# Performance work log

Measured on AMD Instinct MI355X. Metric: run time of the kernel, lower is better.

The kernel has to match this reference:

```python
import jax, jax.numpy as jnp
import numpy as np

B_, C_, H_, W_ = 8, 128, 64, 64
OUT_ = 128
D_MODEL = C_ // 4        # 32, per-chunk channels fed to Mamba
D_STATE = 16
D_CONV = 4
D_INNER = 2 * D_MODEL    # expand=2 -> 64
DT_RANK = max(1, -(-D_MODEL // 16))  # ceil(32/16)=2
SE_RED = 2


def _ln(x, g, b):
    m = x.mean(-1, keepdims=True)
    v = jnp.var(x, axis=-1, keepdims=True)
    return (x - m) / jnp.sqrt(v + 1e-5) * g + b


def _mamba(u, in_W, conv_W, conv_b, xproj_W, dt_W, dt_b, A_log, D_p, out_W):
    # u: (B, L, d_model)
    Bsz, L, _ = u.shape
    xz = u @ in_W.T                                   # (B,L,2*d_inner)
    x, z = jnp.split(xz, 2, axis=-1)
    # causal depthwise conv1d along L
    xc = jnp.swapaxes(x, 1, 2)                        # (B,d_inner,L)
    xc = jax.lax.conv_general_dilated(
        xc, conv_W, (1,), [(D_CONV - 1, 0)],
        feature_group_count=D_INNER,
        dimension_numbers=('NCH', 'OIH', 'NCH'))
    x = jax.nn.silu(jnp.swapaxes(xc + conv_b[None, :, None], 1, 2))
    x_dbl = x @ xproj_W.T                             # (B,L,dt_rank+2*d_state)
    dt, Bm, Cm = jnp.split(x_dbl, [DT_RANK, DT_RANK + D_STATE], axis=-1)
    dt = jax.nn.softplus(dt @ dt_W.T + dt_b)          # (B,L,d_inner)
    A = -jnp.exp(A_log)                               # (d_inner,d_state)
    dA = jnp.exp(dt[..., None] * A)                   # (B,L,d_inner,d_state)
    dBu = dt[..., None] * Bm[:, :, None, :] * x[..., None]

    def step(h, inp):
        dA_t, dBu_t, C_t = inp
        h = dA_t * h + dBu_t                          # (B,d_inner,d_state)
        return h, jnp.einsum('bds,bs->bd', h, C_t)

    h0 = jnp.zeros((Bsz, D_INNER, D_STATE), dtype=x.dtype)
    _, ys = jax.lax.scan(step, h0, (jnp.swapaxes(dA, 0, 1), jnp.swapaxes(dBu, 0, 1), jnp.swapaxes(Cm, 0, 1)))
    y = jnp.swapaxes(ys, 0, 1) + x * D_p
    y = y * jax.nn.silu(z)
    return y @ out_W.T


def _branch(xi, skip_scale, se_W1, se_W2, mp):
    M1 = _mamba(xi, *mp)                              # (B,L,c)
    M2 = skip_scale * xi
    # SE: adaptive avg-pool over spatial == mean over tokens; cat over channels
    y = jnp.concatenate([M1, M2], axis=-1).mean(axis=1)   # (B,2c)
    y = jax.nn.sigmoid(jax.nn.relu(y @ se_W1.T) @ se_W2.T)
    g1, g2 = jnp.split(y, 2, axis=-1)
    return g1[:, None, :] * M1 + g2[:, None, :] * M2


def _pvm(x, norm_g, norm_b, proj_W, proj_b, skip_scale, se_W1, se_W2,
         in_W, conv_W, conv_b, xproj_W, dt_W, dt_b, A_log, D_p, out_W):
    B, C, H, W = x.shape
    L = H * W
    xf = jnp.swapaxes(x.reshape(B, C, L), 1, 2)       # (B,L,C)
    xn = _ln(xf, norm_g, norm_b)
    mp = (in_W, conv_W, conv_b, xproj_W, dt_W, dt_b, A_log, D_p, out_W)
    outs = [_branch(c, skip_scale, se_W1, se_W2, mp) for c in jnp.split(xn, 4, axis=2)]
    xm = jnp.concatenate(outs, axis=2)                # (B,L,C)
    xm = _ln(xm, norm_g, norm_b)
    xm = xm @ proj_W.T + proj_b                       # (B,L,out)
    return jnp.swapaxes(xm, 1, 2).reshape(B, proj_W.shape[0], H, W)


def setup_inputs():
    key = jax.random.key(0)
    ks = jax.random.split(key, 10)
    p = {}
    p['x'] = jax.random.normal(ks[0], (B_, C_, H_, W_), jnp.float32)
    p['norm_g'] = jnp.ones((C_,), jnp.float32)
    p['norm_b'] = jnp.zeros((C_,), jnp.float32)
    p['proj_W'] = jax.random.normal(ks[1], (OUT_, C_), jnp.float32) * 0.05
    p['proj_b'] = jnp.zeros((OUT_,), jnp.float32)
    p['skip_scale'] = jnp.ones((1,), jnp.float32)
    p['se_W1'] = jax.random.normal(ks[2], (SE_RED, 2 * D_MODEL), jnp.float32) * 0.1
    p['se_W2'] = jax.random.normal(ks[3], (2 * D_MODEL, SE_RED), jnp.float32) * 0.1
    p['in_W'] = jax.random.normal(ks[4], (2 * D_INNER, D_MODEL), jnp.float32) * 0.1
    p['conv_W'] = jax.random.normal(ks[5], (D_INNER, 1, D_CONV), jnp.float32) * 0.2
    p['conv_b'] = jnp.zeros((D_INNER,), jnp.float32)
    p['xproj_W'] = jax.random.normal(ks[6], (DT_RANK + 2 * D_STATE, D_INNER), jnp.float32) * 0.1
    p['dt_W'] = jax.random.normal(ks[7], (D_INNER, DT_RANK), jnp.float32) * 0.1
    p['dt_b'] = jnp.full((D_INNER,), -4.6, jnp.float32)  # softplus(-4.6) ~ 0.01 init dt
    p['A_log'] = jnp.log(jnp.broadcast_to(jnp.arange(1.0, D_STATE + 1.0, dtype=jnp.float32), (D_INNER, D_STATE)))
    p['D_p'] = jnp.ones((D_INNER,), jnp.float32)
    p['out_W'] = jax.random.normal(ks[8], (D_MODEL, D_INNER), jnp.float32) * 0.1
    return p


def reference(x, norm_g, norm_b, proj_W, proj_b, skip_scale, se_W1, se_W2,
              in_W, conv_W, conv_b, xproj_W, dt_W, dt_b, A_log, D_p, out_W):
    return _pvm(x, norm_g, norm_b, proj_W, proj_b, skip_scale, se_W1, se_W2,
                in_W, conv_W, conv_b, xproj_W, dt_W, dt_b, A_log, D_p, out_W)
```

## Files before the change

### kernel.cpp

```cpp
#include <hip/hip_runtime.h>
#include <math.h>

typedef _Float16 h16;

#define DEV static __device__ __forceinline__

constexpr int B_ = 8, C_ = 128, L_ = 4096, OUT_ = 128;
constexpr int NCH = 4, DM = 32, DS = 16, DI = 64;
constexpr int NI = 32;
constexpr int NSEG = 128;
constexpr int SL = L_ / NSEG;

DEV float sigmoidf_(float x) { return 1.f / (1.f + __expf(-x)); }
DEV float siluf_(float x) { return x * sigmoidf_(x); }
DEV float softplusf_(float x) { return (x > 20.f) ? x : __logf(1.f + __expf(x)); }

template <int CTRL>
DEV float dpp_add_(float x) {
  int v = __builtin_amdgcn_update_dpp(0, __float_as_int(x), CTRL, 0xf, 0xf, false);
  return x + __int_as_float(v);
}

typedef __attribute__((ext_vector_type(8))) _Float16 f16x8;
typedef __attribute__((ext_vector_type(4))) _Float16 f16x4;
typedef __attribute__((ext_vector_type(4))) float f32x4;

DEV void powladder_(float E, float* out) {
  float E2 = E * E;
  float E4 = E2 * E2;
  float E8 = E4 * E4;
  float E3 = E2 * E;
  out[0] = E;       out[1] = E2;      out[2] = E3;      out[3] = E4;
  out[4] = E4 * E;  out[5] = E4 * E2; out[6] = E4 * E3; out[7] = E8;
  out[8] = E8 * E;  out[9] = E8 * E2; out[10] = E8 * E3; out[11] = E8 * E4;
  out[12] = E8 * out[4]; out[13] = E8 * out[5]; out[14] = E8 * out[6];
  out[15] = E8 * E8;
}

__global__ __launch_bounds__(256) void k1_ln(const float* __restrict__ x,
                                             const float* __restrict__ gn,
                                             const float* __restrict__ bn,
                                             float* __restrict__ XN,
                                             float* __restrict__ SUMXN) {
  int bid = blockIdx.x;
  int b = bid >> 6, tile = bid & 63;
  int t0 = tile * 64;
  int tid = threadIdx.x;
  __shared__ float xT[128][65];
  __shared__ float gnS[128], bnS[128];
  __shared__ float red[256];
  if (tid < 128) { gnS[tid] = gn[tid]; bnS[tid] = bn[tid]; }
  for (int k = tid; k < 8192; k += 256) {
    int c = k >> 6, tt = k & 63;
    xT[c][tt] = x[((size_t)(b * C_ + c)) * L_ + t0 + tt];
  }
  __syncthreads();
  {
    int tok = tid >> 2, q = tid & 3;
    float s = 0.f, qq = 0.f;
#pragma unroll
    for (int j = 0; j < 32; ++j) {
      float v = xT[q + 4 * j][tok];
      s += v; qq += v * v;
    }
    s = dpp_add_<0xB1>(s); qq = dpp_add_<0xB1>(qq);
    s = dpp_add_<0x4E>(s); qq = dpp_add_<0x4E>(qq);
    float m = s * (1.f / 128.f);
    float var = qq * (1.f / 128.f) - m * m;
    float rs = rsqrtf(var + 1e-5f);
#pragma unroll
    for (int j = 0; j < 32; ++j) {
      int c = q + 4 * j;
      float v = xT[c][tok];
      xT[c][tok] = (v - m) * rs * gnS[c] + bnS[c];
    }
  }
  __syncthreads();
  float acc = 0.f;
  int cfix = tid & 127;
  for (int k = tid; k < 8192; k += 256) {
    int tt = k >> 7, c = k & 127;
    float v = xT[c][tt];
    XN[((size_t)(b * L_ + t0 + tt)) * C_ + c] = v;
    acc += v;
  }
  red[tid] = acc;
  __syncthreads();
  if (tid < 128) atomicAdd(&SUMXN[b * C_ + cfix], red[tid] + red[tid + 128]);
}

__global__ __launch_bounds__(256) void k2_prep(
    const float* __restrict__ in_W, const float* __restrict__ conv_W,
    const float* __restrict__ conv_b, const float* __restrict__ xproj_W,
    const float* __restrict__ dt_W, const float* __restrict__ dt_b,
    const float* __restrict__ XN, h16* __restrict__ SX2, h16* __restrict__ SDT2,
    h16* __restrict__ SB2, h16* __restrict__ SC2, h16* __restrict__ SZ2) {
  int bid = blockIdx.x;
  int i = bid >> 6, tile = bid & 63;
  int b = i >> 2, ch = i & 3;
  int t0 = tile * 64;
  int tid = threadIdx.x;
  int w = __builtin_amdgcn_readfirstlane(tid >> 6);
  int lane = tid & 63;

  __shared__ __attribute__((aligned(16))) union {
    struct {
      _Float16 uH[80][40];
      _Float16 w1H[64][40];
    } s;
    float xdS[64][36];
    _Float16 zL[64][88];
  } U;
  __shared__ __attribute__((aligned(16))) _Float16 preH[80][66];
  __shared__ __attribute__((aligned(16))) _Float16 xH[64][72];
  __shared__ __attribute__((aligned(16))) _Float16 w2H[48][72];
  __shared__ float convWS[64][4];
  __shared__ float dtWS[64][2];
  __shared__ float dtbS[64], cbS[64];

  convWS[tid >> 2][tid & 3] = conv_W[tid];
  if (tid < 128) dtWS[tid >> 1][tid & 1] = dt_W[tid];
  if (tid < 64) { dtbS[tid] = dt_b[tid]; cbS[tid] = conv_b[tid]; }
  const float* xn = XN + (size_t)b * L_ * C_ + ch * DM;
  for (int k = tid; k < 80 * 32; k += 256) {
    int r = k >> 5, c = k & 31;
    int tg = t0 - 3 + r;
    float v = (r < 67 && tg >= 0) ? xn[(size_t)tg * C_ + c] : 0.f;
    U.s.uH[r][c] = (_Float16)v;
  }
  for (int k = tid; k < 2048; k += 256) U.s.w1H[k >> 5][k & 31] = (_Float16)in_W[k];
  for (int k = tid; k < 48 * 64; k += 256) {
    int r = k >> 6, c = k & 63;
    w2H[r][c] = (r < 34) ? (_Float16)xproj_W[r * 64 + c] : (_Float16)0.f;
  }
  __syncthreads();

  int rsel = lane & 15, ksel = (lane >> 4) * 8;
  {
    int nt = w;
    f16x8 bf = *(const f16x8*)&U.s.w1H[nt * 16 + rsel][ksel];
    int row0q = (lane >> 4) << 2;
    int col = nt * 16 + rsel;
#pragma unroll
    for (int mt = 0; mt < 5; ++mt) {
      f16x8 af = *(const f16x8*)&U.s.uH[mt * 16 + rsel][ksel];
      f32x4 acc = {0.f, 0.f, 0.f, 0.f};
      acc = __builtin_amdgcn_mfma_f32_16x16x32_f16(af, bf, acc, 0, 0, 0);
      int row0 = mt * 16 + row0q;
#pragma unroll
      for (int r = 0; r < 4; ++r) preH[row0 + r][col] = (_Float16)acc[r];
    }
  }
  f32x4 zacc[4];
  {
    f16x8 bf = *(const f16x8*)&U.s.uH[3 + w * 16 + rsel][ksel];
#pragma unroll
    for (int mt = 0; mt < 4; ++mt) {
      const float* wp = in_W + (64 + mt * 16 + rsel) * 32 + ksel;
      float4 w0 = *(const float4*)wp;
      float4 w1 = *(const float4*)(wp + 4);
      f16x8 af;
      af[0] = (_Float16)w0.x; af[1] = (_Float16)w0.y;
      af[2] = (_Float16)w0.z; af[3] = (_Float16)w0.w;
      af[4] = (_Float16)w1.x; af[5] = (_Float16)w1.y;
      af[6] = (_Float16)w1.z; af[7] = (_Float16)w1.w;
      f32x4 acc = {0.f, 0.f, 0.f, 0.f};
      zacc[mt] = __builtin_amdgcn_mfma_f32_16x16x32_f16(af, bf, acc, 0, 0, 0);
    }
  }
  __syncthreads();

  h16* SXp = SX2 + ((size_t)i * L_ + t0) * DI;
  for (int k = tid; k < 4096; k += 256) {
    int r = k >> 6, d = k & 63;
    float v = cbS[d];
#pragma unroll
    for (int j = 0; j < 4; ++j) v = fmaf(convWS[d][j], (float)preH[r + j][d], v);
    v = siluf_(v);
    xH[r][d] = (_Float16)v;
    SXp[(size_t)r * DI + d] = (h16)v;
  }
  __syncthreads();

  {
    int mt = w;
    f16x8 a0 = *(const f16x8*)&xH[mt * 16 + rsel][ksel];
    f16x8 a1 = *(const f16x8*)&xH[mt * 16 + rsel][32 + ksel];
    int row0 = mt * 16 + ((lane >> 4) << 2);
#pragma unroll
    for (int nt = 0; nt < 3; ++nt) {
      f16x8 b0 = *(const f16x8*)&w2H[nt * 16 + rsel][ksel];
      f16x8 b1 = *(const f16x8*)&w2H[nt * 16 + rsel][32 + ksel];
      f32x4 acc = {0.f, 0.f, 0.f, 0.f};
      acc = __builtin_amdgcn_mfma_f32_16x16x32_f16(a0, b0, acc, 0, 0, 0);
      acc = __builtin_amdgcn_mfma_f32_16x16x32_f16(a1, b1, acc, 0, 0, 0);
      int col = nt * 16 + rsel;
      if (col < 34) {
#pragma unroll
        for (int r = 0; r < 4; ++r) U.xdS[row0 + r][col] = acc[r];
      }
    }
  }
  __syncthreads();

  h16* SDTp = SDT2 + ((size_t)i * L_ + t0) * DI;
  for (int k = tid; k < 4096; k += 256) {
    int d = k & 63, r = k >> 6;
    float raw = fmaf(U.xdS[r][0], dtWS[d][0], fmaf(U.xdS[r][1], dtWS[d][1], dtbS[d]));
    SDTp[(size_t)r * DI + d] = (h16)softplusf_(raw);
  }
  h16* SBp = SB2 + ((size_t)i * L_ + t0) * DS;
  h16* SCp = SC2 + ((size_t)i * L_ + t0) * DS;
  for (int k = tid; k < 1024; k += 256) {
    int s = k & 15, r = k >> 4;
    SBp[(size_t)r * DS + s] = (h16)U.xdS[r][2 + s];
    SCp[(size_t)r * DS + s] = (h16)U.xdS[r][18 + s];
  }
  __syncthreads();

  {
    int tok = w * 16 + rsel;
    int zq = (lane >> 4) << 2;
#pragma unroll
    for (int mt = 0; mt < 4; ++mt) {
      f16x4 pk;
#pragma unroll
      for (int r = 0; r < 4; ++r) pk[r] = (_Float16)siluf_(zacc[mt][r]);
      *(f16x4*)&U.zL[tok][mt * 16 + zq] = pk;
    }
  }
  __syncthreads();
  h16* SZp = SZ2 + ((size_t)i * L_ + t0) * DI;
  for (int k = tid; k < 512; k += 256) {
    int r = k >> 3, dblk = (k & 7) * 8;
    f16x8 v = *(const f16x8*)&U.zL[r][dblk];
    *(f16x8*)&SZp[(size_t)r * DI + dblk] = v;
  }
}

__global__ __launch_bounds__(256) void k3a_seg(
    const float* __restrict__ A_log, const h16* __restrict__ SDT2,
    const h16* __restrict__ SX2, const h16* __restrict__ SB2,
    float* __restrict__ Pp, float* __restrict__ Qp) {
  int bid = blockIdx.x;
  int i = bid >> 5, sg = bid & 31;
  int tid = threadIdx.x;
  int w = tid >> 6, lane = tid & 63;
  int seg = sg * 4 + w;
  int t0 = seg * SL;
  __shared__ float bS[4][SL][20];
  {
    int tk = lane & 31, hf = lane >> 5;
    const h16* pb = SB2 + ((size_t)i * L_ + t0 + tk) * DS + hf * 8;
    float4 r0 = *(const float4*)pb;
    const h16* h0p = (const h16*)&r0;
#pragma unroll
    for (int s = 0; s < 8; ++s) bS[w][tk][hf * 8 + s] = (float)h0p[s];
  }
  __syncthreads();
  float Av[16];
#pragma unroll
  for (int s = 0; s < 16; ++s) Av[s] = -__expf(A_log[lane * 16 + s]);
  float A0 = Av[0];
  bool okf = true;
#pragma unroll
  for (int s = 0; s < 16; ++s) okf &= fabsf(Av[s] - (float)(s + 1) * A0) <= 1e-4f * fabsf(Av[s]);
  int fastp = __all(okf ? 1 : 0);
  float h[16];
#pragma unroll
  for (int s = 0; s < 16; ++s) h[s] = 0.f;
  float sdt = 0.f;
  const h16* pdt = SDT2 + ((size_t)i * L_ + t0) * DI + lane;
  const h16* pxx = SX2 + ((size_t)i * L_ + t0) * DI + lane;
  float dtc = (float)pdt[0], xvc = (float)pxx[0];
  for (int t = 0; t < SL; ++t) {
    float dt = dtc, xv = xvc;
    if (t < SL - 1) { dtc = (float)pdt[(t + 1) * DI]; xvc = (float)pxx[(t + 1) * DI]; }
    float Bv[16];
    const float* row = &bS[w][t][0];
#pragma unroll
    for (int j = 0; j < 4; ++j) *(float4*)&Bv[4 * j] = *(const float4*)(row + 4 * j);
    float dtx = dt * xv;
    float dA[16];
    if (fastp) {
      powladder_(__expf(A0 * dt), dA);
    } else {
#pragma unroll
      for (int s = 0; s < 16; ++s) dA[s] = __expf(Av[s] * dt);
    }
#pragma unroll
    for (int s = 0; s < 16; ++s) h[s] = fmaf(dA[s], h[s], dtx * Bv[s]);
    sdt += dt;
  }
  float P[16];
  if (fastp) {
    powladder_(__expf(A0 * sdt), P);
  } else {
#pragma unroll
    for (int s = 0; s < 16; ++s) P[s] = __expf(Av[s] * sdt);
  }
  size_t base = (((size_t)i * DI + lane) * NSEG + seg) * DS;
#pragma unroll
  for (int j = 0; j < 4; ++j) {
    *(float4*)(Pp + base + 4 * j) = *(float4*)&P[4 * j];
    *(float4*)(Qp + base + 4 * j) = *(float4*)&h[4 * j];
  }
}

__global__ __launch_bounds__(256) void k3b_comb(float* __restrict__ Pp,
                                                const float* __restrict__ Qp) {
  int g = blockIdx.x * 256 + threadIdx.x;
  int s = g & 15;
  int r = g >> 4;
  size_t base = (size_t)r * NSEG * DS + s;
  float H = 0.f;
  for (int seg = 0; seg < NSEG; ++seg) {
    size_t a = base + (size_t)seg * DS;
    float P = Pp[a], Q = Qp[a];
    Pp[a] = H;
    H = fmaf(P, H, Q);
  }
}

__global__ __launch_bounds__(256) void k3c_scan(
    const float* __restrict__ A_log, const h16* __restrict__ SDT2,
    const h16* __restrict__ SX2, const h16* __restrict__ SB2,
    const h16* __restrict__ SC2, const h16* __restrict__ SZ2,
    const float* __restrict__ D_p, const float* __restrict__ H0p,
    h16* __restrict__ YS2, float* __restrict__ SUMYF) {
  int bid = blockIdx.x;
  int i = bid >> 5, sg = bid & 31;
  int tid = threadIdx.x;
  int w = tid >> 6, lane = tid & 63;
  int seg = sg * 4 + w;
  int t0 = seg * SL;
  __shared__ float rowS[4][SL][36];
  {
    int tk = lane & 31, hf = lane >> 5;
    const h16* p = (hf ? SC2 : SB2) + ((size_t)i * L_ + t0 + tk) * DS;
    float4 r0 = *(const float4*)p;
    float4 r1 = *(const float4*)(p + 8);
    const h16* hp0 = (const h16*)&r0;
    const h16* hp1 = (const h16*)&r1;
#pragma unroll
    for (int s = 0; s < 8; ++s) {
      rowS[w][tk][hf * 16 + s] = (float)hp0[s];
      rowS[w][tk][hf * 16 + 8 + s] = (float)hp1[s];
    }
  }
  __syncthreads();
  float Av[16];
#pragma unroll
  for (int s = 0; s < 16; ++s) Av[s] = -__expf(A_log[lane * 16 + s]);
  float A0 = Av[0];
  bool okf = true;
#pragma unroll
  for (int s = 0; s < 16; ++s) okf &= fabsf(Av[s] - (float)(s + 1) * A0) <= 1e-4f * fabsf(Av[s]);
  int fastp = __all(okf ? 1 : 0);
  float Dp = D_p[lane];
  float h[16];
  {
    size_t base = (((size_t)i * DI + lane) * NSEG + seg) * DS;
#pragma unroll
    for (int j = 0; j < 4; ++j) *(float4*)&h[4 * j] = *(const float4*)(H0p + base + 4 * j);
  }
  const h16* pdt = SDT2 + ((size_t)i * L_ + t0) * DI + lane;
  const h16* pxx = SX2 + ((size_t)i * L_ + t0) * DI + lane;
  const h16* pzz = SZ2 + ((size_t)i * L_ + t0) * DI + lane;
  h16* pys = YS2 + ((size_t)i * L_ + t0) * DI + lane;
  float dtc = (float)pdt[0], xvc = (float)pxx[0], zvc = (float)pzz[0];
  float sum = 0.f;
  for (int t = 0; t < SL; ++t) {
    float dt = dtc, xv = xvc, zv = zvc;
    if (t < SL - 1) {
      dtc = (float)pdt[(t + 1) * DI];
      xvc = (float)pxx[(t + 1) * DI];
      zvc = (float)pzz[(t + 1) * DI];
    }
    const float* row = &rowS[w][t][0];
    float Bv[16], Cv[16];
#pragma unroll
    for (int j = 0; j < 4; ++j) {
      *(float4*)&Bv[4 * j] = *(const float4*)(row + 4 * j);
      *(float4*)&Cv[4 * j] = *(const float4*)(row + 16 + 4 * j);
    }
    float dtx = dt * xv;
    float dA[16];
    if (fastp) {
      powladder_(__expf(A0 * dt), dA);
    } else {
#pragma unroll
      for (int s = 0; s < 16; ++s) dA[s] = __expf(Av[s] * dt);
    }
    float y0 = 0.f, y1 = 0.f, y2 = 0.f, y3 = 0.f;
#pragma unroll
    for (int s = 0; s < 16; s += 4) {
      h[s] = fmaf(dA[s], h[s], dtx * Bv[s]);       y0 = fmaf(h[s], Cv[s], y0);
      h[s + 1] = fmaf(dA[s + 1], h[s + 1], dtx * Bv[s + 1]); y1 = fmaf(h[s + 1], Cv[s + 1], y1);
      h[s + 2] = fmaf(dA[s + 2], h[s + 2], dtx * Bv[s + 2]); y2 = fmaf(h[s + 2], Cv[s + 2], y2);
      h[s + 3] = fmaf(dA[s + 3], h[s + 3], dtx * Bv[s + 3]); y3 = fmaf(h[s + 3], Cv[s + 3], y3);
    }
    float y = (y0 + y1) + (y2 + y3);
    float yf = fmaf(xv, Dp, y) * zv;
    pys[(size_t)t * DI] = (h16)yf;
    sum += yf;
  }
  atomicAdd(&SUMYF[i * DI + lane], sum);
}

__global__ __launch_bounds__(64) void k4_gates(
    const float* __restrict__ out_W, const float* __restrict__ se_W1,
    const float* __restrict__ se_W2, const float* __restrict__ skip_p,
    const float* __restrict__ SUMYF, const float* __restrict__ SUMXN,
    float* __restrict__ GATES) {
  int i = blockIdx.x;
  int b = i >> 2, ch = i & 3;
  int tid = threadIdx.x;
  __shared__ float syS[64], catS[64], seS[2];
  syS[tid] = SUMYF[i * DI + tid];
  __syncthreads();
  float invL = 1.f / (float)L_;
  if (tid < 32) {
    float acc = 0.f;
#pragma unroll
    for (int dd = 0; dd < 64; ++dd) acc = fmaf(syS[dd], out_W[tid * 64 + dd], acc);
    catS[tid] = acc * invL;
  } else {
    int c = tid - 32;
    catS[tid] = skip_p[0] * SUMXN[b * C_ + ch * DM + c] * invL;
  }
  __syncthreads();
  if (tid < 2) {
    float acc = 0.f;
#pragma unroll
    for (int k = 0; k < 64; ++k) acc = fmaf(catS[k], se_W1[tid * 64 + k], acc);
    seS[tid] = fmaxf(acc, 0.f);
  }
  __syncthreads();
  float gg = fmaf(seS[0], se_W2[tid * 2 + 0], seS[1] * se_W2[tid * 2 + 1]);
  GATES[i * DI + tid] = sigmoidf_(gg);
}

__global__ __launch_bounds__(256) void k5b_combine(
    const float* __restrict__ out_W, const float* __restrict__ skip_p,
    const float* __restrict__ GATES, const h16* __restrict__ YS2,
    float* __restrict__ XN) {
  int bid = blockIdx.x;
  int i = bid >> 6, tile = bid & 63;
  int b = i >> 2, ch = i & 3;
  int t0 = tile * 64;
  int tid = threadIdx.x;
  int w = __builtin_amdgcn_readfirstlane(tid >> 6);
  int lane = tid & 63;
  __shared__ __attribute__((aligned(16))) _Float16 yH[64][72];
  __shared__ __attribute__((aligned(16))) _Float16 owH[32][72];
  __shared__ float xnS[64][37];
  __shared__ float gS[64];
  if (tid < 64) gS[tid] = GATES[i * DI + tid];
  const h16* py = YS2 + ((size_t)i * L_ + t0) * DI;
  for (int k = tid; k < 512; k += 256) {
    int tt = k >> 3, dblk = (k & 7) * 8;
    *(f16x8*)&yH[tt][dblk] = *(const f16x8*)&py[(size_t)tt * DI + dblk];
  }
  for (int k = tid; k < 2048; k += 256) owH[k >> 6][k & 63] = (_Float16)out_W[k];
  float* xn = XN + (size_t)b * L_ * C_ + ch * DM;
  for (int k = tid; k < 2048; k += 256) {
    int tt = k >> 5, o = k & 31;
    xnS[tt][o] = xn[(size_t)(t0 + tt) * C_ + o];
  }
  __syncthreads();
  int rsel = lane & 15, ksel = (lane >> 4) * 8;
  float skip = skip_p[0];
  int mt = w;
  f16x8 a0 = *(const f16x8*)&yH[mt * 16 + rsel][ksel];
  f16x8 a1 = *(const f16x8*)&yH[mt * 16 + rsel][32 + ksel];
  int row0 = mt * 16 + ((lane >> 4) << 2);
#pragma unroll
  for (int nt = 0; nt < 2; ++nt) {
    f16x8 b0 = *(const f16x8*)&owH[nt * 16 + rsel][ksel];
    f16x8 b1 = *(const f16x8*)&owH[nt * 16 + rsel][32 + ksel];
    f32x4 acc = {0.f, 0.f, 0.f, 0.f};
    acc = __builtin_amdgcn_mfma_f32_16x16x32_f16(a0, b0, acc, 0, 0, 0);
    acc = __builtin_amdgcn_mfma_f32_16x16x32_f16(a1, b1, acc, 0, 0, 0);
    int o = nt * 16 + rsel;
    float g1 = gS[o], g2s = gS[32 + o] * skip;
#pragma unroll
    for (int r = 0; r < 4; ++r) {
      int tok = row0 + r;
      xnS[tok][o] = g1 * acc[r] + g2s * xnS[tok][o];
    }
  }
  __syncthreads();
  for (int k = tid; k < 2048; k += 256) {
    int tt = k >> 5, o = k & 31;
    xn[(size_t)(t0 + tt) * C_ + o] = xnS[tt][o];
  }
}

__global__ __launch_bounds__(256) void k6_ln_proj(
    const float* __restrict__ gn, const float* __restrict__ bn,
    const float* __restrict__ proj_W, const float* __restrict__ proj_b,
    const float* __restrict__ XN, float* __restrict__ out) {
  int bid = blockIdx.x;
  int b = bid >> 6, tile = bid & 63;
  int t0 = tile * 64;
  int tid = threadIdx.x;
  int w = __builtin_amdgcn_readfirstlane(tid >> 6);
  int lane = tid & 63;
  __shared__ __attribute__((aligned(16))) union {
    float xmS[64][132];
    _Float16 projH[128][136];
  } U;
  __shared__ __attribute__((aligned(16))) _Float16 xmH[64][136];
  __shared__ float gnS[128], bnS[128];
  if (tid < 128) { gnS[tid] = gn[tid]; bnS[tid] = bn[tid]; }
  const float* xm = XN + (size_t)b * L_ * C_;
  for (int k = tid; k < 8192; k += 256) {
    int tt = k >> 7, c = k & 127;
    U.xmS[tt][c] = xm[(size_t)(t0 + tt) * C_ + c];
  }
  __syncthreads();
  {
    int tok = tid >> 2, q = tid & 3;
    float s = 0.f, qq = 0.f;
#pragma unroll
    for (int j = 0; j < 32; ++j) {
      float v = U.xmS[tok][4 * j + q];
      s += v; qq += v * v;
    }
    s = dpp_add_<0xB1>(s); qq = dpp_add_<0xB1>(qq);
    s = dpp_add_<0x4E>(s); qq = dpp_add_<0x4E>(qq);
    float m = s * (1.f / 128.f);
    float var = qq * (1.f / 128.f) - m * m;
    float rs = rsqrtf(var + 1e-5f);
#pragma unroll
    for (int j = 0; j < 32; ++j) {
      int c = 4 * j + q;
      float v = U.xmS[tok][c];
      U.xmS[tok][c] = (v - m) * rs * gnS[c] + bnS[c];
    }
  }
  __syncthreads();
  for (int k = tid; k < 1024; k += 256) {
    int tt = k >> 4, cblk = (k & 15) * 8;
    float4 v0 = *(const float4*)&U.xmS[tt][cblk];
    float4 v1 = *(const float4*)&U.xmS[tt][cblk + 4];
    f16x8 hv;
    hv[0] = (_Float16)v0.x; hv[1] = (_Float16)v0.y;
    hv[2] = (_Float16)v0.z; hv[3] = (_Float16)v0.w;
    hv[4] = (_Float16)v1.x; hv[5] = (_Float16)v1.y;
    hv[6] = (_Float16)v1.z; hv[7] = (_Float16)v1.w;
    *(f16x8*)&xmH[tt][cblk] = hv;
  }
  __syncthreads();
  for (int k = tid; k < 2048; k += 256) {
    int o = k >> 4, cblk = (k & 15) * 8;
    const float* wp = proj_W + o * 128 + cblk;
    float4 v0 = *(const float4*)wp;
    float4 v1 = *(const float4*)(wp + 4);
    f16x8 hv;
    hv[0] = (_Float16)v0.x; hv[1] = (_Float16)v0.y;
    hv[2] = (_Float16)v0.z; hv[3] = (_Float16)v0.w;
    hv[4] = (_Float16)v1.x; hv[5] = (_Float16)v1.y;
    hv[6] = (_Float16)v1.z; hv[7] = (_Float16)v1.w;
    *(f16x8*)&U.projH[o][cblk] = hv;
  }
  __syncthreads();
  int rsel = lane & 15, ksel = (lane >> 4) * 8;
  int mt = w;
  f16x8 af[4];
#pragma unroll
  for (int kc = 0; kc < 4; ++kc)
    af[kc] = *(const f16x8*)&xmH[mt * 16 + rsel][kc * 32 + ksel];
  int row0 = mt * 16 + ((lane >> 4) << 2);
#pragma unroll
  for (int nt = 0; nt < 8; ++nt) {
    int o = nt * 16 + rsel;
    float pb = proj_b[o];
    f32x4 acc = {pb, pb, pb, pb};
#pragma unroll
    for (int kc = 0; kc < 4; ++kc) {
      f16x8 bf = *(const f16x8*)&U.projH[o][kc * 32 + ksel];
      acc = __builtin_amdgcn_mfma_f32_16x16x32_f16(af[kc], bf, acc, 0, 0, 0);
    }
    *(float4*)&out[((size_t)(b * OUT_ + o)) * L_ + t0 + row0] =
        make_float4(acc[0], acc[1], acc[2], acc[3]);
  }
}

extern "C" void kernel_launch(void* const* d_in, const int* in_sizes, int n_in,
                              void* d_out, int out_size, void* d_ws, size_t ws_size,
                              hipStream_t stream) {
  const float* x = (const float*)d_in[0];
  const float* norm_g = (const float*)d_in[1];
  const float* norm_b = (const float*)d_in[2];
  const float* proj_W = (const float*)d_in[3];
  const float* proj_b = (const float*)d_in[4];
  const float* skip = (const float*)d_in[5];
  const float* se_W1 = (const float*)d_in[6];
  const float* se_W2 = (const float*)d_in[7];
  const float* in_W = (const float*)d_in[8];
  const float* conv_W = (const float*)d_in[9];
  const float* conv_b = (const float*)d_in[10];
  const float* xproj_W = (const float*)d_in[11];
  const float* dt_W = (const float*)d_in[12];
  const float* dt_b = (const float*)d_in[13];
  const float* A_log = (const float*)d_in[14];
  const float* D_p = (const float*)d_in[15];
  const float* out_W = (const float*)d_in[16];
  float* out = (float*)d_out;

  float* XN = (float*)d_ws;
  float* SUMYF = XN + (size_t)B_ * L_ * C_;
  float* SUMXN = SUMYF + NI * DI;
  float* GATES = SUMXN + B_ * C_;
  float* Pp = GATES + NI * DI;
  float* Qp = Pp + (size_t)NI * DI * NSEG * DS;
  h16* YS2 = (h16*)(Qp + (size_t)NI * DI * NSEG * DS);
  h16* SX2 = YS2 + (size_t)NI * L_ * DI;
  h16* SDT2 = SX2 + (size_t)NI * L_ * DI;
  h16* SB2 = SDT2 + (size_t)NI * L_ * DI;
  h16* SC2 = SB2 + (size_t)NI * L_ * DS;
  h16* SZ2 = SC2 + (size_t)NI * L_ * DS;

  hipMemsetAsync(SUMYF, 0, (size_t)(NI * DI + B_ * C_) * sizeof(float), stream);
  k1_ln<<<B_ * 64, 256, 0, stream>>>(x, norm_g, norm_b, XN, SUMXN);
  k2_prep<<<NI * 64, 256, 0, stream>>>(in_W, conv_W, conv_b, xproj_W, dt_W, dt_b,
                                       XN, SX2, SDT2, SB2, SC2, SZ2);
  k3a_seg<<<NI * 32, 256, 0, stream>>>(A_log, SDT2, SX2, SB2, Pp, Qp);
  k3b_comb<<<128, 256, 0, stream>>>(Pp, Qp);
  k3c_scan<<<NI * 32, 256, 0, stream>>>(A_log, SDT2, SX2, SB2, SC2, SZ2, D_p,
                                        Pp, YS2, SUMYF);
  k4_gates<<<NI, 64, 0, stream>>>(out_W, se_W1, se_W2, skip, SUMYF, SUMXN, GATES);
  k5b_combine<<<NI * 64, 256, 0, stream>>>(out_W, skip, GATES, YS2, XN);
  k6_ln_proj<<<B_ * 64, 256, 0, stream>>>(norm_g, norm_b, proj_W, proj_b, XN, out);
}
```

Baseline: 242.2 us.

## Fuse segment-scan into prep kernel and pre-convert weights and inputs to fp16

The per-segment scan (formerly k3a_seg) now runs inside k2_prep using dt, x and B values already held in shared memory. Each wave handles one segment and half of the state dimension, which removes a kernel launch and the global re-reads of SDT/SX/SB. A new k0_wcvt kernel converts weights to fp16 once, and k1_ln also writes an fp16 copy of the normalized input, so k2 can use vectorized f16x8 loads. The costs are extra shared memory in k2, an extra fp16 output write in k1, and a serial scan added to the end of the prep kernel.

New measurement: 226.3 us. 6.5% less time.

```diff
diff --git a/kernel.cpp b/kernel.cpp
--- a/kernel.cpp
+++ b/kernel.cpp
@@ -37,10 +37,31 @@
   out[15] = E8 * E8;
 }
 
+DEV void powladder8_(float E, float* out) {
+  float E2 = E * E, E3 = E2 * E, E4 = E2 * E2;
+  out[0] = E; out[1] = E2; out[2] = E3; out[3] = E4;
+  out[4] = E4 * E; out[5] = E4 * E2; out[6] = E4 * E3; out[7] = E4 * E4;
+}
+
+__global__ __launch_bounds__(256) void k0_wcvt(const float* __restrict__ in_W,
+                                               const float* __restrict__ xproj_W,
+                                               h16* __restrict__ WH) {
+  int tid = blockIdx.x * 256 + threadIdx.x;
+  if (tid < 4096) {
+    WH[tid] = (h16)in_W[tid];
+  } else {
+    int j = tid - 4096;
+    int r = j >> 6;
+    WH[tid] = (r < 34) ? (h16)xproj_W[j - (r - (r < 34 ? 0 : 0)) * 0 + (r * 64 + (j & 63)) - j + j] : (h16)0.f;
+    WH[tid] = (r < 34) ? (h16)xproj_W[r * 64 + (j & 63)] : (h16)0.f;
+  }
+}
+
 __global__ __launch_bounds__(256) void k1_ln(const float* __restrict__ x,
                                              const float* __restrict__ gn,
                                              const float* __restrict__ bn,
                                              float* __restrict__ XN,
+                                             h16* __restrict__ XNH,
                                              float* __restrict__ SUMXN) {
   int bid = blockIdx.x;
   int b = bid >> 6, tile = bid & 63;
@@ -84,17 +105,25 @@
     XN[((size_t)(b * L_ + t0 + tt)) * C_ + c] = v;
     acc += v;
   }
+  for (int k = tid; k < 1024; k += 256) {
+    int tt = k >> 4, c8 = (k & 15) * 8;
+    f16x8 hv;
+#pragma unroll
+    for (int j = 0; j < 8; ++j) hv[j] = (_Float16)xT[c8 + j][tt];
+    *(f16x8*)&XNH[((size_t)(b * L_ + t0 + tt)) * C_ + c8] = hv;
+  }
   red[tid] = acc;
   __syncthreads();
   if (tid < 128) atomicAdd(&SUMXN[b * C_ + cfix], red[tid] + red[tid + 128]);
 }
 
 __global__ __launch_bounds__(256) void k2_prep(
-    const float* __restrict__ in_W, const float* __restrict__ conv_W,
-    const float* __restrict__ conv_b, const float* __restrict__ xproj_W,
-    const float* __restrict__ dt_W, const float* __restrict__ dt_b,
-    const float* __restrict__ XN, h16* __restrict__ SX2, h16* __restrict__ SDT2,
-    h16* __restrict__ SB2, h16* __restrict__ SC2, h16* __restrict__ SZ2) {
+    const h16* __restrict__ WH, const float* __restrict__ conv_W,
+    const float* __restrict__ conv_b, const float* __restrict__ dt_W,
+    const float* __restrict__ dt_b, const float* __restrict__ A_log,
+    const h16* __restrict__ XNH, h16* __restrict__ SX2, h16* __restrict__ SDT2,
+    h16* __restrict__ SB2, h16* __restrict__ SC2, h16* __restrict__ SZ2,
+    float* __restrict__ Pp, float* __restrict__ Qp) {
   int bid = blockIdx.x;
   int i = bid >> 6, tile = bid & 63;
   int b = i >> 2, ch = i & 3;
@@ -111,6 +140,7 @@
     float xdS[64][36];
     _Float16 zL[64][88];
   } U;
+  __shared__ __attribute__((aligned(16))) _Float16 wzH[64][40];
   __shared__ __attribute__((aligned(16))) _Float16 preH[80][66];
   __shared__ __attribute__((aligned(16))) _Float16 xH[64][72];
   __shared__ __attribute__((aligned(16))) _Float16 w2H[48][72];
@@ -121,17 +151,22 @@
   convWS[tid >> 2][tid & 3] = conv_W[tid];
   if (tid < 128) dtWS[tid >> 1][tid & 1] = dt_W[tid];
   if (tid < 64) { dtbS[tid] = dt_b[tid]; cbS[tid] = conv_b[tid]; }
-  const float* xn = XN + (size_t)b * L_ * C_ + ch * DM;
-  for (int k = tid; k < 80 * 32; k += 256) {
-    int r = k >> 5, c = k & 31;
+  const h16* xnh = XNH + (size_t)b * L_ * C_ + ch * DM;
+  for (int k = tid; k < 320; k += 256) {
+    int r = k >> 2, c8 = (k & 3) * 8;
     int tg = t0 - 3 + r;
-    float v = (r < 67 && tg >= 0) ? xn[(size_t)tg * C_ + c] : 0.f;
-    U.s.uH[r][c] = (_Float16)v;
-  }
-  for (int k = tid; k < 2048; k += 256) U.s.w1H[k >> 5][k & 31] = (_Float16)in_W[k];
-  for (int k = tid; k < 48 * 64; k += 256) {
-    int r = k >> 6, c = k & 63;
-    w2H[r][c] = (r < 34) ? (_Float16)xproj_W[r * 64 + c] : (_Float16)0.f;
+    f16x8 v = {0, 0, 0, 0, 0, 0, 0, 0};
+    if (r < 67 && tg >= 0) v = *(const f16x8*)&xnh[(size_t)tg * C_ + c8];
+    *(f16x8*)&U.s.uH[r][c8] = v;
+  }
+  if (tid < 256) {
+    int r = tid >> 2, c8 = (tid & 3) * 8;
+    *(f16x8*)&U.s.w1H[r][c8] = *(const f16x8*)&WH[r * 32 + c8];
+    *(f16x8*)&wzH[r][c8] = *(const f16x8*)&WH[(64 + r) * 32 + c8];
+  }
+  for (int k = tid; k < 384; k += 256) {
+    int r = k >> 3, c8 = (k & 7) * 8;
+    *(f16x8*)&w2H[r][c8] = *(const f16x8*)&WH[4096 + r * 64 + c8];
   }
   __syncthreads();
 
@@ -156,14 +191,7 @@
     f16x8 bf = *(const f16x8*)&U.s.uH[3 + w * 16 + rsel][ksel];
 #pragma unroll
     for (int mt = 0; mt < 4; ++mt) {
-      const float* wp = in_W + (64 + mt * 16 + rsel) * 32 + ksel;
-      float4 w0 = *(const float4*)wp;
-      float4 w1 = *(const float4*)(wp + 4);
-      f16x8 af;
-      af[0] = (_Float16)w0.x; af[1] = (_Float16)w0.y;
-      af[2] = (_Float16)w0.z; af[3] = (_Float16)w0.w;
-      af[4] = (_Float16)w1.x; af[5] = (_Float16)w1.y;
-      af[6] = (_Float16)w1.z; af[7] = (_Float16)w1.w;
+      f16x8 af = *(const f16x8*)&wzH[mt * 16 + rsel][ksel];
       f32x4 acc = {0.f, 0.f, 0.f, 0.f};
       zacc[mt] = __builtin_amdgcn_mfma_f32_16x16x32_f16(af, bf, acc, 0, 0, 0);
     }
@@ -203,11 +231,14 @@
   }
   __syncthreads();
 
+  h16* dtL = (h16*)&preH[0][0];
   h16* SDTp = SDT2 + ((size_t)i * L_ + t0) * DI;
   for (int k = tid; k < 4096; k += 256) {
     int d = k & 63, r = k >> 6;
     float raw = fmaf(U.xdS[r][0], dtWS[d][0], fmaf(U.xdS[r][1], dtWS[d][1], dtbS[d]));
-    SDTp[(size_t)r * DI + d] = (h16)softplusf_(raw);
+    float dtv = softplusf_(raw);
+    dtL[r * 66 + d] = (_Float16)dtv;
+    SDTp[(size_t)r * DI + d] = (h16)dtv;
   }
   h16* SBp = SB2 + ((size_t)i * L_ + t0) * DS;
   h16* SCp = SC2 + ((size_t)i * L_ + t0) * DS;
@@ -219,6 +250,66 @@
   __syncthreads();
 
   {
+    int seg = w >> 1, shalf = w & 1;
+    int s0 = shalf * 8;
+    float Av[16];
+#pragma unroll
+    for (int s = 0; s < 16; ++s) Av[s] = -__expf(A_log[lane * 16 + s]);
+    float A0 = Av[0];
+    bool okf = true;
+#pragma unroll
+    for (int s = 0; s < 16; ++s)
+      okf &= fabsf(Av[s] - (float)(s + 1) * A0) <= 1e-4f * fabsf(Av[s]);
+    int fastp = __all(okf ? 1 : 0);
+    float h[8];
+#pragma unroll
+    for (int j = 0; j < 8; ++j) h[j] = 0.f;
+    float sdt = 0.f;
+    int rowbase = seg * SL;
+    for (int t = 0; t < SL; ++t) {
+      int row = rowbase + t;
+      float dt = (float)dtL[row * 66 + lane];
+      float xv = (float)xH[row][lane];
+      float dtx = dt * xv;
+      float dA[8];
+      if (fastp) {
+        powladder8_(__expf(A0 * dt), dA);
+        if (shalf) {
+          float E8 = dA[7];
+#pragma unroll
+          for (int j = 0; j < 8; ++j) dA[j] *= E8;
+        }
+      } else {
+#pragma unroll
+        for (int j = 0; j < 8; ++j) dA[j] = __expf(Av[s0 + j] * dt);
+      }
+      const float* brow = &U.xdS[row][2 + s0];
+#pragma unroll
+      for (int j = 0; j < 8; ++j) h[j] = fmaf(dA[j], h[j], dtx * brow[j]);
+      sdt += dt;
+    }
+    float P[8];
+    if (fastp) {
+      powladder8_(__expf(A0 * sdt), P);
+      if (shalf) {
+        float E8 = P[7];
+#pragma unroll
+        for (int j = 0; j < 8; ++j) P[j] *= E8;
+      }
+    } else {
+#pragma unroll
+      for (int j = 0; j < 8; ++j) P[j] = __expf(Av[s0 + j] * sdt);
+    }
+    int segg = tile * 2 + seg;
+    size_t base = (((size_t)i * DI + lane) * NSEG + segg) * DS + s0;
+    *(float4*)(Pp + base) = *(float4*)&P[0];
+    *(float4*)(Pp + base + 4) = *(float4*)&P[4];
+    *(float4*)(Qp + base) = *(float4*)&h[0];
+    *(float4*)(Qp + base + 4) = *(float4*)&h[4];
+  }
+  __syncthreads();
+
+  {
     int tok = w * 16 + rsel;
     int zq = (lane >> 4) << 2;
 #pragma unroll
@@ -235,75 +326,6 @@
     int r = k >> 3, dblk = (k & 7) * 8;
     f16x8 v = *(const f16x8*)&U.zL[r][dblk];
     *(f16x8*)&SZp[(size_t)r * DI + dblk] = v;
-  }
-}
-
-__global__ __launch_bounds__(256) void k3a_seg(
-    const float* __restrict__ A_log, const h16* __restrict__ SDT2,
-    const h16* __restrict__ SX2, const h16* __restrict__ SB2,
-    float* __restrict__ Pp, float* __restrict__ Qp) {
-  int bid = blockIdx.x;
-  int i = bid >> 5, sg = bid & 31;
-  int tid = threadIdx.x;
-  int w = tid >> 6, lane = tid & 63;
-  int seg = sg * 4 + w;
-  int t0 = seg * SL;
-  __shared__ float bS[4][SL][20];
-  {
-    int tk = lane & 31, hf = lane >> 5;
-    const h16* pb = SB2 + ((size_t)i * L_ + t0 + tk) * DS + hf * 8;
-    float4 r0 = *(const float4*)pb;
-    const h16* h0p = (const h16*)&r0;
-#pragma unroll
-    for (int s = 0; s < 8; ++s) bS[w][tk][hf * 8 + s] = (float)h0p[s];
-  }
-  __syncthreads();
-  float Av[16];
-#pragma unroll
-  for (int s = 0; s < 16; ++s) Av[s] = -__expf(A_log[lane * 16 + s]);
-  float A0 = Av[0];
-  bool okf = true;
-#pragma unroll
-  for (int s = 0; s < 16; ++s) okf &= fabsf(Av[s] - (float)(s + 1) * A0) <= 1e-4f * fabsf(Av[s]);
-  int fastp = __all(okf ? 1 : 0);
-  float h[16];
-#pragma unroll
-  for (int s = 0; s < 16; ++s) h[s] = 0.f;
-  float sdt = 0.f;
-  const h16* pdt = SDT2 + ((size_t)i * L_ + t0) * DI + lane;
-  const h16* pxx = SX2 + ((size_t)i * L_ + t0) * DI + lane;
-  float dtc = (float)pdt[0], xvc = (float)pxx[0];
-  for (int t = 0; t < SL; ++t) {
-    float dt = dtc, xv = xvc;
-    if (t < SL - 1) { dtc = (float)pdt[(t + 1) * DI]; xvc = (float)pxx[(t + 1) * DI]; }
-    float Bv[16];
-    const float* row = &bS[w][t][0];
-#pragma unroll
-    for (int j = 0; j < 4; ++j) *(float4*)&Bv[4 * j] = *(const float4*)(row + 4 * j);
-    float dtx = dt * xv;
-    float dA[16];
-    if (fastp) {
-      powladder_(__expf(A0 * dt), dA);
-    } else {
-#pragma unroll
-      for (int s = 0; s < 16; ++s) dA[s] = __expf(Av[s] * dt);
-    }
-#pragma unroll
-    for (int s = 0; s < 16; ++s) h[s] = fmaf(dA[s], h[s], dtx * Bv[s]);
-    sdt += dt;
-  }
-  float P[16];
-  if (fastp) {
-    powladder_(__expf(A0 * sdt), P);
-  } else {
-#pragma unroll
-    for (int s = 0; s < 16; ++s) P[s] = __expf(Av[s] * sdt);
-  }
-  size_t base = (((size_t)i * DI + lane) * NSEG + seg) * DS;
-#pragma unroll
-  for (int j = 0; j < 4; ++j) {
-    *(float4*)(Pp + base + 4 * j) = *(float4*)&P[4 * j];
-    *(float4*)(Qp + base + 4 * j) = *(float4*)&h[4 * j];
   }
 }
 
@@ -622,12 +644,14 @@
   h16* SB2 = SDT2 + (size_t)NI * L_ * DI;
   h16* SC2 = SB2 + (size_t)NI * L_ * DS;
   h16* SZ2 = SC2 + (size_t)NI * L_ * DS;
+  h16* XNH = SZ2 + (size_t)NI * L_ * DI;
+  h16* WH = XNH + (size_t)B_ * L_ * C_;
 
   hipMemsetAsync(SUMYF, 0, (size_t)(NI * DI + B_ * C_) * sizeof(float), stream);
-  k1_ln<<<B_ * 64, 256, 0, stream>>>(x, norm_g, norm_b, XN, SUMXN);
-  k2_prep<<<NI * 64, 256, 0, stream>>>(in_W, conv_W, conv_b, xproj_W, dt_W, dt_b,
-                                       XN, SX2, SDT2, SB2, SC2, SZ2);
-  k3a_seg<<<NI * 32, 256, 0, stream>>>(A_log, SDT2, SX2, SB2, Pp, Qp);
+  k0_wcvt<<<28, 256, 0, stream>>>(in_W, xproj_W, WH);
+  k1_ln<<<B_ * 64, 256, 0, stream>>>(x, norm_g, norm_b, XN, XNH, SUMXN);
+  k2_prep<<<NI * 64, 256, 0, stream>>>(WH, conv_W, conv_b, dt_W, dt_b, A_log,
+                                       XNH, SX2, SDT2, SB2, SC2, SZ2, Pp, Qp);
   k3b_comb<<<128, 256, 0, stream>>>(Pp, Qp);
   k3c_scan<<<NI * 32, 256, 0, stream>>>(A_log, SDT2, SX2, SB2, SC2, SZ2, D_p,
                                         Pp, YS2, SUMYF);
```
